# Performance work log

Measured on AMD Instinct MI355X. Metric: run time of the kernel, lower is better.

The kernel has to match this reference:

```python
import jax, jax.numpy as jnp
import numpy as np

D_MODEL = 768
D_VERTEX = 32
TEMPERATURE = 1.0
ADJ_W = 0.1
SPEC_W = 0.1
EPS = 1e-8
LN_EPS = 1e-5


def _cube_buffers():
    # 64 vertices of the 6D hypercube, bit patterns (64, 6)
    bits = ((np.arange(64)[:, None] >> np.arange(6)[None, :]) & 1).astype(np.float32)
    ham = (bits[:, None, :] != bits[None, :, :]).sum(-1)
    adj = (ham == 1).astype(np.float32) * 0.5          # adjacency * 0.5 (register_cube_buffers)
    spec = 2.0 * bits - 1.0                             # (64, 6) spectral embedding
    ap = bits[:, 0]                                     # aperture subcube mask
    bd = bits[:, 1]                                     # boundary subcube mask
    rs = bits[:, 2]                                     # resonance subcube mask
    return adj, spec, ap, bd, rs


def setup_inputs() -> dict:
    key = jax.random.key(0)
    ks = jax.random.split(key, 16)
    B, S, D, DV = 2, 1024, D_MODEL, D_VERTEX
    d3 = D // 3
    x = jax.random.normal(ks[0], (B, S, D), dtype=jnp.float32)
    causal = jnp.tril(jnp.ones((S, S), dtype=jnp.float32))
    mask = jnp.broadcast_to(causal, (B, S, S))
    sc = 0.02
    Wq = jax.random.normal(ks[1], (DV, D), dtype=jnp.float32) * sc
    Wk = jax.random.normal(ks[2], (DV, D), dtype=jnp.float32) * sc
    vertex_emb = jax.random.normal(ks[3], (64, DV), dtype=jnp.float32) * sc
    vertex_gates = jax.random.normal(ks[4], (64, D), dtype=jnp.float32) * sc
    Wv = jax.random.normal(ks[5], (D, D), dtype=jnp.float32) * sc
    Wspec = jax.random.normal(ks[6], (DV, 6), dtype=jnp.float32) * sc
    Wa = jax.random.normal(ks[7], (d3, D), dtype=jnp.float32) * sc
    Wb = jax.random.normal(ks[8], (d3, D), dtype=jnp.float32) * sc
    Wr = jax.random.normal(ks[9], (D - 2 * d3, D), dtype=jnp.float32) * sc
    Wo = jax.random.normal(ks[10], (D, D), dtype=jnp.float32) * sc
    bo = jnp.zeros((D,), dtype=jnp.float32)
    gamma = jnp.ones((D,), dtype=jnp.float32)
    beta = jnp.zeros((D,), dtype=jnp.float32)
    adj, spec, ap, bd, rs = _cube_buffers()
    return {
        'x': x, 'mask': mask, 'Wq': Wq, 'Wk': Wk, 'vertex_emb': vertex_emb,
        'vertex_gates': vertex_gates, 'Wv': Wv, 'Wspec': Wspec,
        'Wa': Wa, 'Wb': Wb, 'Wr': Wr, 'Wo': Wo, 'bo': bo,
        'gamma': gamma, 'beta': beta,
        'adj_bias': jnp.asarray(adj), 'spectral_emb': jnp.asarray(spec),
        'ap_mask': jnp.asarray(ap), 'bd_mask': jnp.asarray(bd), 'rs_mask': jnp.asarray(rs),
    }


def reference(x, mask, Wq, Wk, vertex_emb, vertex_gates, Wv, Wspec, Wa, Wb, Wr,
              Wo, bo, gamma, beta, adj_bias, spectral_emb, ap_mask, bd_mask, rs_mask):
    q = x @ Wq.T                                   # (B,S,DV)
    k = x @ Wk.T                                   # (B,S,DV)
    inter = q[:, :, None, :] * k[:, None, :, :]    # (B,S,S,DV)
    # fuse vertex + spectral projections: inter@(E + sw*spec_proj).T
    spec_proj = spectral_emb @ Wspec.T             # (64, DV)
    emb = vertex_emb + SPEC_W * spec_proj          # (64, DV)
    s = jnp.einsum('bijd,vd->bijv', inter, emb)    # (B,S,S,64)
    # fuse adjacency bias: s + aw*(s@A) = s @ (I + aw*A)
    M = jnp.eye(64, dtype=s.dtype) + ADJ_W * adj_bias
    v_scores = s @ M
    pi = jax.nn.softmax(v_scores / TEMPERATURE, axis=-1)
    pi = pi * mask[..., None]

    gate_mean = jax.nn.sigmoid(vertex_gates).mean(axis=-1)   # (64,)
    scalar_attn = jnp.einsum('bijv,v->bij', pi, gate_mean)
    scalar_attn = scalar_attn / (scalar_attn.sum(-1, keepdims=True) + EPS)
    out = scalar_attn @ (x @ Wv.T)                 # (B,S,D)

    def modal(smask, W):
        mp = jnp.einsum('bijv,v->bij', pi, smask)
        mp = mp / (mp.sum(-1, keepdims=True) + EPS)
        mp = mp * mask
        mp = mp / (mp.sum(-1, keepdims=True) + EPS)
        return mp @ (x @ W.T)

    modal_out = jnp.concatenate(
        [modal(ap_mask, Wa), modal(bd_mask, Wb), modal(rs_mask, Wr)], axis=-1)
    combined = out + modal_out
    result = combined @ Wo.T + bo
    mu = result.mean(-1, keepdims=True)
    var = result.var(-1, keepdims=True)
    normed = (result - mu) * jax.lax.rsqrt(var + LN_EPS) * gamma + beta
    return normed, pi
```

## Files before the change

### kernel.cpp

```cpp
#include <hip/hip_runtime.h>

typedef unsigned short u16;
typedef unsigned int u32;
typedef __bf16 bf16x8 __attribute__((ext_vector_type(8)));
typedef float f32x4 __attribute__((ext_vector_type(4)));

#define S_LEN 1024
#define D_MODEL 768
#define N_CONV 19
#define BORROW_ROW 1888

__device__ __forceinline__ float bf2f(u16 h) {
    u32 u = ((u32)h) << 16;
    return __builtin_bit_cast(float, u);
}
__device__ __forceinline__ u16 f2bf(float f) {
    u32 u = __builtin_bit_cast(u32, f);
    u32 r = (u + 0x7fffu + ((u >> 16) & 1u)) >> 16;
    return (u16)r;
}
__device__ __forceinline__ float ldin(const void* p, long long i, bool isbf) {
    return isbf ? bf2f(((const u16*)p)[i]) : ((const float*)p)[i];
}

struct ConvArgs {
    const void* src[N_CONV];
    int n[N_CONV];
    int off[N_CONV];
};

__global__ __launch_bounds__(256) void k0_kernel(
    ConvArgs a, u16* __restrict__ dst, const u16* __restrict__ probe,
    const void* __restrict__ vemb, const void* __restrict__ vgates,
    const void* __restrict__ Wspec, const void* __restrict__ adj,
    const void* __restrict__ spec, const void* __restrict__ ap,
    const void* __restrict__ bd, const void* __restrict__ rs,
    u16* __restrict__ emb2bf, float* __restrict__ w4)
{
    bool isbf = (probe[0] == 0x3F80u);
    int inp = blockIdx.y;
    if (inp < N_CONV) {
        int n = a.n[inp];
        u16* d = dst + a.off[inp];
        const u16* s16 = (const u16*)a.src[inp];
        const float* s32 = (const float*)a.src[inp];
        int base = blockIdx.x * 1024 + threadIdx.x;
#pragma unroll
        for (int t = 0; t < 4; ++t) {
            int idx = base + t * 256;
            if (idx < n) d[idx] = isbf ? s16[idx] : f2bf(s32[idx]);
        }
        return;
    }
    if (blockIdx.x != 0) return;
    __shared__ float emb[64 * 32];
    __shared__ float gred[256];
    int tid = threadIdx.x;
    for (int p = 0; p < 8; ++p) {
        int idx = tid + p * 256;
        int v = idx >> 5, d = idx & 31;
        float acc = ldin(vemb, idx, isbf);
        for (int t = 0; t < 6; ++t)
            acc += 0.1f * ldin(spec, v * 6 + t, isbf) * ldin(Wspec, d * 6 + t, isbf);
        emb[idx] = acc;
    }
    __syncthreads();
    for (int p = 0; p < 8; ++p) {
        int idx = tid + p * 256;
        int u = idx >> 5, d = idx & 31;
        float a2 = 0.f;
        for (int v = 0; v < 64; ++v)
            a2 += ldin(adj, v * 64 + u, isbf) * emb[v * 32 + d];
        emb2bf[idx] = f2bf(emb[idx] + 0.1f * a2);
    }
    int u = tid >> 2, qp = tid & 3;
    float acc = 0.f;
    for (int c = 0; c < 192; ++c) {
        float x = ldin(vgates, u * 768 + qp * 192 + c, isbf);
        acc += 1.f / (1.f + __expf(-x));
    }
    gred[tid] = acc;
    __syncthreads();
    if (qp == 0) {
        float gm = (gred[tid] + gred[tid + 1] + gred[tid + 2] + gred[tid + 3]) * (1.f / 768.f);
        w4[u * 4 + 0] = gm;
        w4[u * 4 + 1] = ldin(ap, u, isbf);
        w4[u * 4 + 2] = ldin(bd, u, isbf);
        w4[u * 4 + 3] = ldin(rs, u, isbf);
    }
}

template <int KC, int OUT_BF16>
__device__ __forceinline__ void gemm_body(
    const u16* __restrict__ A, const u16* __restrict__ B,
    void* __restrict__ C, int ldc, int m0, int n0, int lane)
{
    int quad = lane >> 4, l16 = lane & 15;
    f32x4 acc[2][2] = {};
#pragma unroll 2
    for (int k0 = 0; k0 < KC; k0 += 32) {
        bf16x8 a[2], b[2];
#pragma unroll
        for (int mi = 0; mi < 2; ++mi)
            a[mi] = *reinterpret_cast<const bf16x8*>(A + (long long)(m0 + mi * 16 + l16) * KC + k0 + quad * 8);
#pragma unroll
        for (int ni = 0; ni < 2; ++ni)
            b[ni] = *reinterpret_cast<const bf16x8*>(B + (long long)(n0 + ni * 16 + l16) * KC + k0 + quad * 8);
#pragma unroll
        for (int mi = 0; mi < 2; ++mi)
#pragma unroll
            for (int ni = 0; ni < 2; ++ni)
                acc[mi][ni] = __builtin_amdgcn_mfma_f32_16x16x32_bf16(a[mi], b[ni], acc[mi][ni], 0, 0, 0);
    }
#pragma unroll
    for (int mi = 0; mi < 2; ++mi)
#pragma unroll
        for (int ni = 0; ni < 2; ++ni) {
            int col = n0 + ni * 16 + l16;
#pragma unroll
            for (int r = 0; r < 4; ++r) {
                int row = m0 + mi * 16 + quad * 4 + r;
                if (OUT_BF16)
                    ((u16*)C)[(long long)row * ldc + col] = f2bf(acc[mi][ni][r]);
                else
                    ((float*)C)[(long long)row * ldc + col] = acc[mi][ni][r];
            }
        }
}

__global__ __launch_bounds__(256) void gemm_qkvx_kernel(
    const u16* __restrict__ xb, const u16* __restrict__ Wqkb,
    const u16* __restrict__ WvAllb, u16* __restrict__ VX2, float* __restrict__ qk)
{
    int lane = threadIdx.x & 63;
    int wave = threadIdx.x >> 6;
    int z = blockIdx.z;
    if (z < 2) {
        int m0 = blockIdx.x * 64 + (wave >> 1) * 32;
        int n0 = blockIdx.y * 64 + (wave & 1) * 32;
        gemm_body<768, 1>(WvAllb, xb + (long long)z * S_LEN * D_MODEL,
                          VX2 + (long long)z * 1536 * S_LEN, S_LEN, m0, n0, lane);
    } else {
        int t = blockIdx.y * 24 + blockIdx.x;
        if (t >= 32) return;
        int m0 = t * 64 + (wave >> 1) * 32;
        int n0 = (wave & 1) * 32;
        gemm_body<768, 0>(xb, Wqkb, qk, 64, m0, n0, lane);
    }
}

__global__ __launch_bounds__(256) void gemm_f_kernel(
    const u16* __restrict__ combb, const u16* __restrict__ Wob, u16* __restrict__ resf)
{
    int lane = threadIdx.x & 63;
    int wave = threadIdx.x >> 6;
    int m0 = blockIdx.x * 64 + (wave >> 1) * 32;
    int n0 = blockIdx.y * 64 + (wave & 1) * 32;
    gemm_body<768, 1>(combb, Wob, resf, 768, m0, n0, lane);
}

__global__ __launch_bounds__(256) void efused_kernel(
    const u16* __restrict__ wpl, const u16* __restrict__ VX2,
    const float* __restrict__ scl, u16* __restrict__ combb)
{
    const int S = S_LEN;
    const long long SS = (long long)S * S;
    int b = blockIdx.z;
    int lane = threadIdx.x & 63;
    int wave = threadIdx.x >> 6;
    int quad = lane >> 4, l16 = lane & 15;
    int m0 = blockIdx.x * 64 + (wave >> 1) * 32;
    int n0 = blockIdx.y * 64 + (wave & 1) * 32;
    int g = (blockIdx.y * 64) >> 8;

    const u16* A0 = wpl + (long long)b * 4 * SS;
    const u16* Ag = A0 + (long long)(1 + g) * SS;
    const u16* B = VX2 + (long long)b * 1536 * S;

    f32x4 acc0[2][2] = {}, accg[2][2] = {};
#pragma unroll 2
    for (int k0 = 0; k0 < S; k0 += 32) {
        bf16x8 a0[2], ag[2], b0[2], bg[2];
#pragma unroll
        for (int mi = 0; mi < 2; ++mi) {
            long long r = m0 + mi * 16 + l16;
            a0[mi] = *reinterpret_cast<const bf16x8*>(A0 + r * S + k0 + quad * 8);
            ag[mi] = *reinterpret_cast<const bf16x8*>(Ag + r * S + k0 + quad * 8);
        }
#pragma unroll
        for (int ni = 0; ni < 2; ++ni) {
            long long c = n0 + ni * 16 + l16;
            b0[ni] = *reinterpret_cast<const bf16x8*>(B + c * S + k0 + quad * 8);
            bg[ni] = *reinterpret_cast<const bf16x8*>(B + (768 + c) * S + k0 + quad * 8);
        }
#pragma unroll
        for (int mi = 0; mi < 2; ++mi)
#pragma unroll
            for (int ni = 0; ni < 2; ++ni) {
                acc0[mi][ni] = __builtin_amdgcn_mfma_f32_16x16x32_bf16(a0[mi], b0[ni], acc0[mi][ni], 0, 0, 0);
                accg[mi][ni] = __builtin_amdgcn_mfma_f32_16x16x32_bf16(ag[mi], bg[ni], accg[mi][ni], 0, 0, 0);
            }
    }
    const float* s0p = scl + (long long)(b * 4) * S;
    const float* sgp = scl + (long long)(b * 4 + 1 + g) * S;
#pragma unroll
    for (int mi = 0; mi < 2; ++mi)
#pragma unroll
        for (int ni = 0; ni < 2; ++ni) {
            int col = n0 + ni * 16 + l16;
#pragma unroll
            for (int r = 0; r < 4; ++r) {
                int row = m0 + mi * 16 + quad * 4 + r;
                float v = s0p[row] * acc0[mi][ni][r] + sgp[row] * accg[mi][ni][r];
                combb[(long long)b * S * D_MODEL + (long long)row * D_MODEL + col] = f2bf(v);
            }
        }
}

template <int MODE>
__global__ __launch_bounds__(256) void stage_c_kernel(
    const float* __restrict__ qk,
    const u16* __restrict__ emb2bf,
    const float* __restrict__ w4,
    float* __restrict__ pi_out, u16* __restrict__ wpl, float* __restrict__ scales,
    int pi_limit)
{
    const int S = S_LEN;
    const long long SS = (long long)S * S;
    int grow = MODE ? (BORROW_ROW + (int)blockIdx.x) : (int)blockIdx.x;
    int b = grow >> 10, i = grow & 1023;
    bool write_pi = MODE ? true : (grow < pi_limit);
    int tid = threadIdx.x;
    int lane = tid & 63, wave = tid >> 6;
    int quad = lane >> 4, l16 = lane & 15;

    bf16x8 afrag[4];
#pragma unroll
    for (int mi = 0; mi < 4; ++mi)
        afrag[mi] = *reinterpret_cast<const bf16x8*>(emb2bf + (mi * 16 + l16) * 32 + quad * 8);

    const float* qp = qk + (long long)grow * 64 + quad * 8;
    f32x4 q0 = *(const f32x4*)qp;
    f32x4 q1 = *(const f32x4*)(qp + 4);

    f32x4 w4r[4][4];
    if (MODE == 0) {
#pragma unroll
        for (int mi = 0; mi < 4; ++mi)
#pragma unroll
            for (int r = 0; r < 4; ++r)
                w4r[mi][r] = *(const f32x4*)(w4 + (mi * 16 + quad * 4 + r) * 4);
    }

    float* pirow = pi_out + (long long)grow * (S * 64);
    const float* kb = qk + ((long long)(b << 10)) * 64;
    u16* wrow = wpl + (long long)(b * 4 + quad) * SS + (long long)i * S;

    float rs = 0.f;

    for (int t = wave; t < 64; t += 4) {
        int j0 = t << 4;
        int jl = j0 + l16;
        float* pdst = pirow + (long long)jl * 64 + quad * 4;
        if (j0 > i) {
            if (write_pi) {
                f32x4 z = {0.f, 0.f, 0.f, 0.f};
#pragma unroll
                for (int mi = 0; mi < 4; ++mi) *(f32x4*)(pdst + mi * 16) = z;
            }
            if (MODE == 0) wrow[jl] = 0;
            continue;
        }
        const float* kp = kb + (long long)jl * 64 + 32 + quad * 8;
        f32x4 k0 = *(const f32x4*)kp;
        f32x4 k1 = *(const f32x4*)(kp + 4);
        bf16x8 bfr;
#pragma unroll
        for (int d = 0; d < 4; ++d) bfr[d] = (__bf16)(k0[d] * q0[d]);
#pragma unroll
        for (int d = 0; d < 4; ++d) bfr[4 + d] = (__bf16)(k1[d] * q1[d]);

        f32x4 acc[4];
#pragma unroll
        for (int mi = 0; mi < 4; ++mi) {
            f32x4 z = {0.f, 0.f, 0.f, 0.f};
            acc[mi] = __builtin_amdgcn_mfma_f32_16x16x32_bf16(afrag[mi], bfr, z, 0, 0, 0);
        }
        float sum = 0.f;
        f32x4 pg = {0.f, 0.f, 0.f, 0.f};
        float e[4][4];
#pragma unroll
        for (int mi = 0; mi < 4; ++mi)
#pragma unroll
            for (int r = 0; r < 4; ++r) {
                float ev = __expf(acc[mi][r]);
                e[mi][r] = ev;
                sum += ev;
                if (MODE == 0) pg += w4r[mi][r] * ev;
            }
        sum += __shfl_xor(sum, 16);
        sum += __shfl_xor(sum, 32);
        if (MODE == 0) {
#pragma unroll
            for (int c = 0; c < 4; ++c) {
                pg[c] += __shfl_xor(pg[c], 16);
                pg[c] += __shfl_xor(pg[c], 32);
            }
        }
        float inv = 1.0f / sum;
        float sc = (jl <= i) ? inv : 0.f;
        if (write_pi) {
#pragma unroll
            for (int mi = 0; mi < 4; ++mi) {
                f32x4 pv;
#pragma unroll
                for (int r = 0; r < 4; ++r) pv[r] = e[mi][r] * sc;
                *(f32x4*)(pdst + mi * 16) = pv;
            }
        }
        if (MODE == 0) {
            float a = pg[quad] * sc;
            wrow[jl] = f2bf(a);
            rs += a;
        }
    }
    if (MODE == 1) return;
    rs += __shfl_xor(rs, 1);
    rs += __shfl_xor(rs, 2);
    rs += __shfl_xor(rs, 4);
    rs += __shfl_xor(rs, 8);
    __shared__ float sred[16];
    if (l16 == 0) sred[wave * 4 + quad] = rs;
    __syncthreads();
    if (tid < 4) {
        float R = sred[tid] + sred[4 + tid] + sred[8 + tid] + sred[12 + tid];
        float scv;
        if (tid == 0) {
            scv = 1.f / (R + 1e-8f);
        } else {
            float T1 = R + 1e-8f;
            float T2 = R / T1 + 1e-8f;
            scv = 1.f / (T1 * T2);
        }
        scales[(b * 4 + tid) * S + i] = scv;
    }
}

__global__ __launch_bounds__(256) void ln_kernel(
    const u16* __restrict__ resf, const u16* __restrict__ bo,
    const u16* __restrict__ gamma, const u16* __restrict__ beta,
    float* __restrict__ out)
{
    int row = blockIdx.x;
    int tid = threadIdx.x;
    __shared__ float red[256];
    float x[3];
#pragma unroll
    for (int p = 0; p < 3; ++p) {
        int c = tid + p * 256;
        x[p] = bf2f(resf[(long long)row * 768 + c]) + bf2f(bo[c]);
    }
    float ls = x[0] + x[1] + x[2];
    red[tid] = ls;
    __syncthreads();
    for (int st = 128; st > 0; st >>= 1) {
        if (tid < st) red[tid] += red[tid + st];
        __syncthreads();
    }
    float mu = red[0] * (1.f / 768.f);
    __syncthreads();
    float ls2 = 0.f;
#pragma unroll
    for (int p = 0; p < 3; ++p) {
        float d = x[p] - mu;
        ls2 += d * d;
    }
    red[tid] = ls2;
    __syncthreads();
    for (int st = 128; st > 0; st >>= 1) {
        if (tid < st) red[tid] += red[tid + st];
        __syncthreads();
    }
    float var = red[0] * (1.f / 768.f);
    float rstd = rsqrtf(var + 1e-5f);
#pragma unroll
    for (int p = 0; p < 3; ++p) {
        int c = tid + p * 256;
        out[(long long)row * 768 + c] = (x[p] - mu) * rstd * bf2f(gamma[c]) + bf2f(beta[c]);
    }
}

extern "C" void kernel_launch(void* const* d_in, const int* in_sizes, int n_in,
                              void* d_out, int out_size, void* d_ws, size_t ws_size,
                              hipStream_t stream)
{
    const long long S = S_LEN, D = D_MODEL, BS = 2 * S;

    float* out_norm = (float*)d_out;
    float* out_pi   = out_norm + BS * D;

    char* wsp = (char*)d_ws;
    size_t woff = 0;
    auto walloc = [&](size_t bytes) -> void* {
        void* p = wsp + woff;
        woff = (woff + bytes + 255) & ~(size_t)255;
        return p;
    };
    u16*   emb2bf = (u16*)walloc(64 * 32 * 2);
    float* w4     = (float*)walloc(64 * 4 * 4);
    float* qkbuf  = (float*)walloc(BS * 64 * 4);
    float* scl    = (float*)walloc(2 * 4 * S * 4);

    static const int cidx[N_CONV] = {0, 2, 3, 6, 8, 9, 10, 4, 5, 7, 11, 12, 13, 14, 15, 16, 17, 18, 19};
    ConvArgs ca;
    int coff[N_CONV];
    long long conv_elems = 0;
    for (int t = 0; t < N_CONV; ++t) {
        ca.src[t] = d_in[cidx[t]];
        ca.n[t] = in_sizes[cidx[t]];
        coff[t] = (int)conv_elems;
        ca.off[t] = (int)conv_elems;
        conv_elems += (in_sizes[cidx[t]] + 127) & ~127;
    }

    long long bulk_elems = ((conv_elems + 127) & ~(long long)127)
                         + 2LL * 1536 * S + 128
                         + BS * D + 128
                         + 2LL * 4 * S * S + 128
                         + BS * D + 128;
    bool usews = (ws_size >= woff + (size_t)bulk_elems * 2 + (1u << 20));

    u16* bulk = usews ? (u16*)(wsp + woff)
                      : (u16*)(out_pi + (long long)BORROW_ROW * S * 64);
    long long boff = 0;
    auto balloc = [&](long long elems) -> u16* {
        u16* p = bulk + boff;
        boff += (elems + 127) & ~(long long)127;
        return p;
    };
    u16* conv  = balloc(conv_elems);
    u16* VX2   = balloc(2 * 1536 * S);
    u16* combb = balloc(BS * D);
    u16* wpl   = balloc(2 * 4 * S * S);
    u16* resf  = balloc(BS * D);

    const u16* xb      = conv + coff[0];
    const u16* Wqkb    = conv + coff[1];
    const u16* WvAllb  = conv + coff[3];
    const u16* Wob     = conv + coff[10];
    const u16* bob     = conv + coff[11];
    const u16* gammab  = conv + coff[12];
    const u16* betab   = conv + coff[13];

    int pi_limit = usews ? 2048 : BORROW_ROW;

    k0_kernel<<<dim3(1536, N_CONV + 1), dim3(256), 0, stream>>>(
        ca, conv, (const u16*)d_in[13],
        d_in[4], d_in[5], d_in[7], d_in[15], d_in[16], d_in[17], d_in[18], d_in[19],
        emb2bf, w4);

    gemm_qkvx_kernel<<<dim3(24, 16, 3), dim3(256), 0, stream>>>(
        xb, Wqkb, WvAllb, VX2, qkbuf);

    stage_c_kernel<0><<<dim3(2048), dim3(256), 0, stream>>>(
        qkbuf, emb2bf, w4, out_pi, wpl, scl, pi_limit);

    efused_kernel<<<dim3(16, 12, 2), dim3(256), 0, stream>>>(wpl, VX2, scl, combb);

    gemm_f_kernel<<<dim3(32, 12), dim3(256), 0, stream>>>(combb, Wob, resf);

    ln_kernel<<<dim3(2048), dim3(256), 0, stream>>>(resf, bob, gammab, betab, out_norm);

    if (!usews) {
        stage_c_kernel<1><<<dim3(2048 - BORROW_ROW), dim3(256), 0, stream>>>(
            qkbuf, emb2bf, w4, out_pi, wpl, scl, 2048);
    }
}
```

Measured before the change: 776.6 us.

## Vectorize conversion and layernorm, enlarge per-wave tile in V projection GEMM

The input conversion kernel now processes 8 elements per thread with vector loads and stores, and its grid shrinks to match. The V/X projection GEMM gives each wave a 64x32 tile instead of 32x32, which halves the grid's y dimension and reuses each A fragment across more MFMAs. Layernorm now handles one row per wave with vector loads and shuffle reductions, replacing the shared-memory tree and its barriers. Conversion assumes every element count is a multiple of 8; any tail elements would be dropped.

```diff
diff --git a/kernel.cpp b/kernel.cpp
--- a/kernel.cpp
+++ b/kernel.cpp
@@ -4,6 +4,8 @@
 typedef unsigned int u32;
 typedef __bf16 bf16x8 __attribute__((ext_vector_type(8)));
 typedef float f32x4 __attribute__((ext_vector_type(4)));
+typedef u16 u16x8 __attribute__((ext_vector_type(8)));
+typedef u16 u16x4 __attribute__((ext_vector_type(4)));
 
 #define S_LEN 1024
 #define D_MODEL 768
@@ -40,15 +42,25 @@
     bool isbf = (probe[0] == 0x3F80u);
     int inp = blockIdx.y;
     if (inp < N_CONV) {
-        int n = a.n[inp];
-        u16* d = dst + a.off[inp];
-        const u16* s16 = (const u16*)a.src[inp];
-        const float* s32 = (const float*)a.src[inp];
+        int nch = a.n[inp] >> 3;
+        u16x8* d = (u16x8*)(dst + a.off[inp]);
+        const u16x8* s16 = (const u16x8*)a.src[inp];
+        const f32x4* s32 = (const f32x4*)a.src[inp];
         int base = blockIdx.x * 1024 + threadIdx.x;
 #pragma unroll
         for (int t = 0; t < 4; ++t) {
-            int idx = base + t * 256;
-            if (idx < n) d[idx] = isbf ? s16[idx] : f2bf(s32[idx]);
+            int c = base + t * 256;
+            if (c < nch) {
+                u16x8 o;
+                if (isbf) {
+                    o = s16[c];
+                } else {
+                    f32x4 lo = s32[c * 2], hi = s32[c * 2 + 1];
+#pragma unroll
+                    for (int e = 0; e < 4; ++e) { o[e] = f2bf(lo[e]); o[4 + e] = f2bf(hi[e]); }
+                }
+                d[c] = o;
+            }
         }
         return;
     }
@@ -128,6 +140,41 @@
         }
 }
 
+template <int KC>
+__device__ __forceinline__ void gemm_body_4x2(
+    const u16* __restrict__ A, const u16* __restrict__ B,
+    u16* __restrict__ C, int ldc, int m0, int n0, int lane)
+{
+    int quad = lane >> 4, l16 = lane & 15;
+    f32x4 acc[4][2] = {};
+#pragma unroll 2
+    for (int k0 = 0; k0 < KC; k0 += 32) {
+        bf16x8 a[4], b[2];
+#pragma unroll
+        for (int mi = 0; mi < 4; ++mi)
+            a[mi] = *reinterpret_cast<const bf16x8*>(A + (long long)(m0 + mi * 16 + l16) * KC + k0 + quad * 8);
+#pragma unroll
+        for (int ni = 0; ni < 2; ++ni)
+            b[ni] = *reinterpret_cast<const bf16x8*>(B + (long long)(n0 + ni * 16 + l16) * KC + k0 + quad * 8);
+#pragma unroll
+        for (int mi = 0; mi < 4; ++mi)
+#pragma unroll
+            for (int ni = 0; ni < 2; ++ni)
+                acc[mi][ni] = __builtin_amdgcn_mfma_f32_16x16x32_bf16(a[mi], b[ni], acc[mi][ni], 0, 0, 0);
+    }
+#pragma unroll
+    for (int mi = 0; mi < 4; ++mi)
+#pragma unroll
+        for (int ni = 0; ni < 2; ++ni) {
+            int col = n0 + ni * 16 + l16;
+#pragma unroll
+            for (int r = 0; r < 4; ++r) {
+                int row = m0 + mi * 16 + quad * 4 + r;
+                C[(long long)row * ldc + col] = f2bf(acc[mi][ni][r]);
+            }
+        }
+}
+
 __global__ __launch_bounds__(256) void gemm_qkvx_kernel(
     const u16* __restrict__ xb, const u16* __restrict__ Wqkb,
     const u16* __restrict__ WvAllb, u16* __restrict__ VX2, float* __restrict__ qk)
@@ -136,10 +183,10 @@
     int wave = threadIdx.x >> 6;
     int z = blockIdx.z;
     if (z < 2) {
-        int m0 = blockIdx.x * 64 + (wave >> 1) * 32;
-        int n0 = blockIdx.y * 64 + (wave & 1) * 32;
-        gemm_body<768, 1>(WvAllb, xb + (long long)z * S_LEN * D_MODEL,
-                          VX2 + (long long)z * 1536 * S_LEN, S_LEN, m0, n0, lane);
+        int m0 = blockIdx.x * 64;
+        int n0 = blockIdx.y * 128 + wave * 32;
+        gemm_body_4x2<768>(WvAllb, xb + (long long)z * S_LEN * D_MODEL,
+                           VX2 + (long long)z * 1536 * S_LEN, S_LEN, m0, n0, lane);
     } else {
         int t = blockIdx.y * 24 + blockIdx.x;
         if (t >= 32) return;
@@ -351,42 +398,46 @@
     const u16* __restrict__ gamma, const u16* __restrict__ beta,
     float* __restrict__ out)
 {
-    int row = blockIdx.x;
-    int tid = threadIdx.x;
-    __shared__ float red[256];
-    float x[3];
+    int lane = threadIdx.x & 63;
+    int wave = threadIdx.x >> 6;
+    int row = blockIdx.x * 4 + wave;
+
+    float x[12];
+    float s = 0.f;
 #pragma unroll
     for (int p = 0; p < 3; ++p) {
-        int c = tid + p * 256;
-        x[p] = bf2f(resf[(long long)row * 768 + c]) + bf2f(bo[c]);
-    }
-    float ls = x[0] + x[1] + x[2];
-    red[tid] = ls;
-    __syncthreads();
-    for (int st = 128; st > 0; st >>= 1) {
-        if (tid < st) red[tid] += red[tid + st];
-        __syncthreads();
-    }
-    float mu = red[0] * (1.f / 768.f);
-    __syncthreads();
-    float ls2 = 0.f;
+        int c = p * 256 + lane * 4;
+        u16x4 xr = *(const u16x4*)(resf + (long long)row * 768 + c);
+        u16x4 br = *(const u16x4*)(bo + c);
+#pragma unroll
+        for (int e = 0; e < 4; ++e) {
+            float v = bf2f(xr[e]) + bf2f(br[e]);
+            x[p * 4 + e] = v;
+            s += v;
+        }
+    }
+#pragma unroll
+    for (int st = 1; st < 64; st <<= 1) s += __shfl_xor(s, st);
+    float mu = s * (1.f / 768.f);
+    float v2 = 0.f;
+#pragma unroll
+    for (int e = 0; e < 12; ++e) {
+        float d = x[e] - mu;
+        v2 += d * d;
+    }
+#pragma unroll
+    for (int st = 1; st < 64; st <<= 1) v2 += __shfl_xor(v2, st);
+    float rstd = rsqrtf(v2 * (1.f / 768.f) + 1e-5f);
 #pragma unroll
     for (int p = 0; p < 3; ++p) {
-        float d = x[p] - mu;
-        ls2 += d * d;
-    }
-    red[tid] = ls2;
-    __syncthreads();
-    for (int st = 128; st > 0; st >>= 1) {
-        if (tid < st) red[tid] += red[tid + st];
-        __syncthreads();
-    }
-    float var = red[0] * (1.f / 768.f);
-    float rstd = rsqrtf(var + 1e-5f);
-#pragma unroll
-    for (int p = 0; p < 3; ++p) {
-        int c = tid + p * 256;
-        out[(long long)row * 768 + c] = (x[p] - mu) * rstd * bf2f(gamma[c]) + bf2f(beta[c]);
+        int c = p * 256 + lane * 4;
+        u16x4 gr = *(const u16x4*)(gamma + c);
+        u16x4 be = *(const u16x4*)(beta + c);
+        f32x4 o;
+#pragma unroll
+        for (int e = 0; e < 4; ++e)
+            o[e] = (x[p * 4 + e] - mu) * rstd * bf2f(gr[e]) + bf2f(be[e]);
+        *(f32x4*)(out + (long long)row * 768 + c) = o;
     }
 }
 
@@ -454,12 +505,12 @@
 
     int pi_limit = usews ? 2048 : BORROW_ROW;
 
-    k0_kernel<<<dim3(1536, N_CONV + 1), dim3(256), 0, stream>>>(
+    k0_kernel<<<dim3(192, N_CONV + 1), dim3(256), 0, stream>>>(
         ca, conv, (const u16*)d_in[13],
         d_in[4], d_in[5], d_in[7], d_in[15], d_in[16], d_in[17], d_in[18], d_in[19],
         emb2bf, w4);
 
-    gemm_qkvx_kernel<<<dim3(24, 16, 3), dim3(256), 0, stream>>>(
+    gemm_qkvx_kernel<<<dim3(24, 8, 3), dim3(256), 0, stream>>>(
         xb, Wqkb, WvAllb, VX2, qkbuf);
 
     stage_c_kernel<0><<<dim3(2048), dim3(256), 0, stream>>>(
@@ -469,7 +520,7 @@
 
     gemm_f_kernel<<<dim3(32, 12), dim3(256), 0, stream>>>(combb, Wob, resf);
 
-    ln_kernel<<<dim3(2048), dim3(256), 0, stream>>>(resf, bob, gammab, betab, out_norm);
+    ln_kernel<<<dim3(512), dim3(256), 0, stream>>>(resf, bob, gammab, betab, out_norm);
 
     if (!usews) {
         stage_c_kernel<1><<<dim3(2048 - BORROW_ROW), dim3(256), 0, stream>>>(
```

Result: faster. 752.1 us (-3.2%).
